# Kernel optimization log

Hardware: AMD Instinct MI355X
Metric: run time of the kernel (lower is better)

## Reference

```python
import jax, jax.numpy as jnp
import numpy as np

N = 2048      # num_nodes
B = 64        # batch
D_IN = 2      # input_dim per node
UNITS = 64    # hidden dim
K = 2         # max_diffusion_step
N_SUP = 2     # dual_random_walk -> two supports
M = N_SUP * K + 1           # num_matrices = 5
IN_SIZE = D_IN + UNITS      # 66
E = 65536                   # nnz per support


def setup_inputs() -> dict:
    key = jax.random.key(0)
    ks = jax.random.split(key, 10)
    inputs = jax.random.normal(ks[0], (B, N * D_IN), jnp.float32)
    state = jax.random.normal(ks[1], (B, N * UNITS), jnp.float32)
    edges1 = jax.random.randint(ks[2], (2, E), 0, N)
    vals1 = jax.random.uniform(ks[3], (E,), jnp.float32) / 32.0  # ~row-stochastic scale
    edges2 = jax.random.randint(ks[4], (2, E), 0, N)
    vals2 = jax.random.uniform(ks[5], (E,), jnp.float32) / 32.0
    W_gate = jax.random.normal(ks[6], (IN_SIZE * M, 2 * UNITS), jnp.float32) * 0.08
    b_gate = jnp.ones((2 * UNITS,), jnp.float32)  # bias_start=1.0 for gate
    W_cand = jax.random.normal(ks[7], (IN_SIZE * M, UNITS), jnp.float32) * 0.08
    b_cand = jnp.zeros((UNITS,), jnp.float32)
    return dict(inputs=inputs, state=state, edges1=edges1, vals1=vals1,
                edges2=edges2, vals2=vals2, W_gate=W_gate, b_gate=b_gate,
                W_cand=W_cand, b_cand=b_cand)


def _spmm(rows, cols, vals, x):
    # sparse [N,N] @ dense [N,F] via gather + segment_sum
    return jax.ops.segment_sum(x[cols] * vals[:, None], rows, num_segments=N)


def _dconv(inp, st, supports, W, b, out_dim):
    # inputs/state -> [B, N, F] concat, F = IN_SIZE
    x = jnp.concatenate([inp.reshape(B, N, -1), st.reshape(B, N, -1)], axis=2)
    f = x.shape[2]
    x0 = x.transpose(1, 2, 0).reshape(N, f * B)  # [N, F*B]
    xs = [x0]
    for (rows, cols, vals) in supports:
        x1 = _spmm(rows, cols, vals, x0)
        xs.append(x1)
        xk_1, xk_2 = x1, x0
        for _ in range(2, K + 1):  # Chebyshev recursion: x_k = 2 S x_{k-1} - x_{k-2}
            xk = 2.0 * _spmm(rows, cols, vals, xk_1) - xk_2
            xs.append(xk)
            xk_1, xk_2 = xk, xk_1
    xcat = jnp.stack(xs, 0).reshape(M, N, f, B)
    xcat = xcat.transpose(3, 1, 2, 0).reshape(B * N, f * M)  # [B*N, F*M]
    out = xcat @ W + b
    return out.reshape(B, N * out_dim)


def reference(inputs, state, edges1, vals1, edges2, vals2, W_gate, b_gate, W_cand, b_cand):
    supports = [(edges1[0], edges1[1], vals1), (edges2[0], edges2[1], vals2)]
    value = jax.nn.sigmoid(_dconv(inputs, state, supports, W_gate, b_gate, 2 * UNITS))
    value = value.reshape(B, N, 2 * UNITS)
    r = value[:, :, :UNITS].reshape(B, N * UNITS)
    u = value[:, :, UNITS:].reshape(B, N * UNITS)
    c = jnp.tanh(_dconv(inputs, r * state, supports, W_cand, b_cand, UNITS))
    new_state = u * state + (1.0 - u) * c
    return new_state
```

## Files before the change

kernel.cpp:

```cpp
#include <hip/hip_runtime.h>
#include <stdint.h>

#define NN 2048
#define EE 65536
#define APITCH 360
#define XSN ((size_t)NN*4096)
#define XIN ((size_t)NN*128)

typedef unsigned short u16;
typedef __bf16 bf16x8 __attribute__((ext_vector_type(8)));
typedef float f32x4 __attribute__((ext_vector_type(4)));
typedef float f32x2 __attribute__((ext_vector_type(2)));
typedef unsigned u32x4 __attribute__((ext_vector_type(4)));

__device__ __forceinline__ float bf2f(u16 h){ return __uint_as_float(((unsigned)h)<<16); }
__device__ __forceinline__ u16 f2bf(float f){
  unsigned u = __float_as_uint(f);
  u += 0x7fffu + ((u>>16)&1u);
  return (u16)(u>>16);
}
__device__ __forceinline__ float loadf(const void* p, size_t i, int bfflag){
  return bfflag ? bf2f(((const u16*)p)[i]) : ((const float*)p)[i];
}
__device__ __forceinline__ f32x2 up2(unsigned u){
  f32x2 r; r.x = __uint_as_float(u<<16); r.y = __uint_as_float(u & 0xffff0000u); return r;
}
__device__ __forceinline__ unsigned pk2(f32x2 t){
  return (unsigned)f2bf(t.x) | ((unsigned)f2bf(t.y)<<16);
}
__device__ __forceinline__ void accv(float v, u32x4 d, f32x2* a){
  f32x2 vv = {v, v};
  a[0] += vv*up2(d.x); a[1] += vv*up2(d.y);
  a[2] += vv*up2(d.z); a[3] += vv*up2(d.w);
}

__global__ void setup1_k(const unsigned* __restrict__ vals,
                         const int* __restrict__ e1, const int* __restrict__ e2,
                         int* __restrict__ cnt, int* __restrict__ flag){
  int b = blockIdx.x, tid = threadIdx.x;
  if (b == 0){
    if (tid < 64){
      unsigned lo = vals[tid] & 0xffffu;
      unsigned long long m = __ballot(lo >= 0x2800u && lo < 0x3D80u);
      if (tid==0) *flag = (__popcll(m) >= 32) ? 1 : 0;
    }
  } else if (b <= 256){
    atomicAdd(&cnt[e1[(b-1)*256 + tid]], 1);
  } else {
    atomicAdd(&cnt[2048 + e2[(b-257)*256 + tid]], 1);
  }
}

__global__ void scan2_k(const int* __restrict__ cntA, int* __restrict__ rpA, int* __restrict__ curA){
  __shared__ int s[1024];
  const int* cnt = cntA + blockIdx.x*2048;
  int* rp  = rpA  + blockIdx.x*2049;
  int* cur = curA + blockIdx.x*2048;
  int t = threadIdx.x;
  int c0 = cnt[2*t], c1 = cnt[2*t+1];
  int ps = c0 + c1;
  s[t] = ps;
  __syncthreads();
  for (int off=1; off<1024; off<<=1){
    int v = (t>=off) ? s[t-off] : 0;
    __syncthreads();
    s[t] += v;
    __syncthreads();
  }
  int excl = s[t] - ps;
  rp[2*t] = excl;  cur[2*t] = excl;
  rp[2*t+1] = excl + c0;  cur[2*t+1] = excl + c0;
  if (t==0) rp[2048] = EE;
}

__global__ void setup2_k(const int* __restrict__ e1, const void* __restrict__ v1,
                         const int* __restrict__ e2, const void* __restrict__ v2,
                         int* __restrict__ curA, int2* __restrict__ scvA,
                         const void* __restrict__ Wg, const void* __restrict__ Wc,
                         u16* __restrict__ Wfg, u16* __restrict__ Wfc,
                         const void* __restrict__ inp, const void* __restrict__ st,
                         u16* __restrict__ XSb, u16* __restrict__ XIb,
                         const int* __restrict__ flag){
  int b = blockIdx.x, tid = threadIdx.x;
  int bfflag = *flag;
  if (b < 512){
    const int* rows; const int* cols; const void* vals; int* cur; int2* scv; int e;
    if (b < 256){ rows=e1; cols=e1+EE; vals=v1; cur=curA; scv=scvA; e=b*256+tid; }
    else { rows=e2; cols=e2+EE; vals=v2; cur=curA+2048; scv=scvA+EE; e=(b-256)*256+tid; }
    int r = rows[e];
    int p = atomicAdd(&cur[r], 1);
    int2 cv; cv.x = cols[e] << 13; cv.y = __float_as_int(loadf(vals, e, bfflag));
    scv[p] = cv;
  } else if (b < 776){
    int bb = b - 512;
    const void* W; u16* Wf; int O, OT, i;
    if (bb < 176){ W=Wg; Wf=Wfg; O=128; OT=8; i=bb*256+tid; }
    else { W=Wc; Wf=Wfc; O=64; OT=4; i=(bb-176)*256+tid; }
    int j = i & 7, L = (i>>3)&63, tq = i>>9;
    int t = tq % OT, q = tq / OT;
    int o = t*16 + (L&15);
    int kk = q*32 + (L>>4)*8 + j;
    float v = 0.f;
    if (kk < 320){ int m = kk>>6, f = (kk&63)+2; v = loadf(W, (size_t)(f*5+m)*O + o, bfflag); }
    else if (kk < 330){ int tt = kk-320; int m = tt>>1, f = tt&1; v = loadf(W, (size_t)(f*5+m)*O + o, bfflag); }
    Wf[i] = f2bf(v);
  } else {
    int n = b - 776;
    if (bfflag){
      const uint4* sp = (const uint4*)st;
      uint4* xp = (uint4*)(XSb + (size_t)n*4096);
      #pragma unroll
      for (int it=0; it<2; ++it){
        int r = tid + it*256;
        int bb = r>>3, v4 = r&7;
        xp[r] = sp[(size_t)bb*(NN*8) + (size_t)n*8 + v4];
      }
      if (tid < 64){
        ((unsigned*)XIb)[n*64 + tid] = ((const unsigned*)inp)[(size_t)tid*NN + n];
      }
    } else {
      for (int i=tid; i<4096; i+=256){
        int bb=i>>6, f=i&63;
        XSb[(size_t)n*4096+i] = f2bf(((const float*)st)[(size_t)bb*(NN*64) + n*64 + f]);
      }
      for (int i=tid; i<128; i+=256){
        int bb=i>>1, f=i&1;
        XIb[(size_t)n*128+i] = f2bf(((const float*)inp)[(size_t)bb*(NN*2) + n*2 + f]);
      }
    }
  }
}

template<int CHEB>
__global__ __launch_bounds__(64) void spmm_k(
    u16* __restrict__ XSb, u16* __restrict__ XIb,
    const int* __restrict__ rpA, const int2* __restrict__ scvA){
  int sup = blockIdx.y;
  const int* rp = rpA + sup*2049;
  const int2* scv = scvA + sup*EE;
  const int srcm = CHEB ? (sup?3:1) : 0;
  const int dstm = CHEB ? (sup?4:2) : (sup?3:1);
  int tid = threadIdx.x;
  int bx = blockIdx.x;
  if (bx < NN*8){
    int ch = bx & 7, n = bx >> 3;
    int e0 = rp[n], e1 = rp[n+1];
    unsigned offB = (unsigned)(ch*64 + tid)*16;
    const char* srcp = (const char*)(XSb + (size_t)srcm*XSN) + offB;
    f32x2 a[4] = {{0.f,0.f},{0.f,0.f},{0.f,0.f},{0.f,0.f}};
    int e = e0;
    for (; e+7 < e1; e += 8){
      const int4* s4 = (const int4*)(scv + e);
      int4 p0 = s4[0], p1 = s4[1], p2 = s4[2], p3 = s4[3];
      u32x4 d0 = *(const u32x4*)(srcp + (unsigned)p0.x);
      u32x4 d1 = *(const u32x4*)(srcp + (unsigned)p0.z);
      u32x4 d2 = *(const u32x4*)(srcp + (unsigned)p1.x);
      u32x4 d3 = *(const u32x4*)(srcp + (unsigned)p1.z);
      u32x4 d4 = *(const u32x4*)(srcp + (unsigned)p2.x);
      u32x4 d5 = *(const u32x4*)(srcp + (unsigned)p2.z);
      u32x4 d6 = *(const u32x4*)(srcp + (unsigned)p3.x);
      u32x4 d7 = *(const u32x4*)(srcp + (unsigned)p3.z);
      accv(__int_as_float(p0.y), d0, a);
      accv(__int_as_float(p0.w), d1, a);
      accv(__int_as_float(p1.y), d2, a);
      accv(__int_as_float(p1.w), d3, a);
      accv(__int_as_float(p2.y), d4, a);
      accv(__int_as_float(p2.w), d5, a);
      accv(__int_as_float(p3.y), d6, a);
      accv(__int_as_float(p3.w), d7, a);
    }
    for (; e < e1; ++e){
      int2 c = scv[e];
      accv(__int_as_float(c.y), *(const u32x4*)(srcp + (unsigned)c.x), a);
    }
    unsigned doff = ((unsigned)n << 13) + offB;
    u32x4 w;
    if (CHEB){
      u32x4 o = *(const u32x4*)((const char*)XSb + doff);
      f32x2 t;
      t = 2.f*a[0] - up2(o.x); w.x = pk2(t);
      t = 2.f*a[1] - up2(o.y); w.y = pk2(t);
      t = 2.f*a[2] - up2(o.z); w.z = pk2(t);
      t = 2.f*a[3] - up2(o.w); w.w = pk2(t);
    } else {
      w.x = pk2(a[0]); w.y = pk2(a[1]); w.z = pk2(a[2]); w.w = pk2(a[3]);
    }
    *(u32x4*)((char*)(XSb + (size_t)dstm*XSN) + doff) = w;
  } else {
    int idx = bx - NN*8;
    int n = idx*2 + (tid>>5), m = tid & 31;
    int e0 = rp[n], e1 = rp[n+1];
    const char* srcp = (const char*)(XIb + (size_t)srcm*XIN) + m*8;
    f32x2 a0 = {0.f,0.f}, a1 = {0.f,0.f};
    for (int e=e0; e<e1; ++e){
      int2 cv = scv[e];
      uint2 d = *(const uint2*)(srcp + ((unsigned)cv.x >> 5));
      f32x2 vv = {__int_as_float(cv.y), __int_as_float(cv.y)};
      a0 += vv*up2(d.x); a1 += vv*up2(d.y);
    }
    unsigned doff = (unsigned)n*256 + m*8;
    if (CHEB){
      uint2 o = *(const uint2*)((const char*)XIb + doff);
      a0 = 2.f*a0 - up2(o.x); a1 = 2.f*a1 - up2(o.y);
    }
    uint2 wv; wv.x = pk2(a0); wv.y = pk2(a1);
    *(uint2*)((char*)(XIb + (size_t)dstm*XIN) + doff) = wv;
  }
}

template<int OT, int MODE>
__global__ __launch_bounds__(256) void gemm_k(
    u16* __restrict__ XSb, const u16* __restrict__ XIb,
    const u16* __restrict__ Wf, const void* __restrict__ bias,
    const void* __restrict__ state, void* __restrict__ outp,
    const int* __restrict__ flag){
  __shared__ __align__(16) u16 A[64*APITCH];
  int tid = threadIdx.x, n = blockIdx.x;
  int bfflag = *flag;
  #pragma unroll
  for (int m=0;m<5;m++){
    const uint4* src = (const uint4*)(XSb + (size_t)m*XSN + ((size_t)n<<12));
    #pragma unroll
    for (int it=0; it<2; ++it){
      int r = tid + it*256;
      uint4 d = src[r];
      int b = r>>3, f0 = (r&7)*8;
      *(uint4*)&A[b*APITCH + m*64 + f0] = d;
    }
  }
  for (int i=tid; i<320; i+=256){
    int m = i>>6, b = i&63;
    unsigned v = ((const unsigned*)XIb)[(size_t)m*(XIN/2) + n*64 + b];
    *(unsigned*)&A[b*APITCH + 320 + 2*m] = v;
  }
  for (int i=tid; i<64*15; i+=256){
    int b = i/15, j = i - b*15;
    *(unsigned*)&A[b*APITCH + 330 + 2*j] = 0;
  }
  const int TW = OT/4;
  int lane = tid & 63, w = tid >> 6;
  int m16 = lane & 15, q4 = lane >> 4;
  const bf16x8* wp = (const bf16x8*)Wf;
  bf16x8 wfr[11][TW];
  #pragma unroll
  for (int q=0;q<11;q++){
    #pragma unroll
    for (int i=0;i<TW;i++) wfr[q][i] = wp[(q*OT + (w + 4*i))*64 + lane];
  }
  __syncthreads();
  #pragma unroll
  for (int rt4=0; rt4<4; ++rt4){
    const u16* arow = A + (rt4*16 + m16)*APITCH + q4*8;
    f32x4 acc[TW];
    #pragma unroll
    for (int i=0;i<TW;i++) acc[i] = (f32x4){0.f,0.f,0.f,0.f};
    #pragma unroll
    for (int q=0;q<11;q++){
      bf16x8 af = *((const bf16x8*)(arow + q*32));
      #pragma unroll
      for (int i=0;i<TW;i++)
        acc[i] = __builtin_amdgcn_mfma_f32_16x16x32_bf16(af, wfr[q][i], acc[i], 0, 0, 0);
    }
    #pragma unroll
    for (int i=0;i<TW;i++){
      int t = w + 4*i;
      int o = t*16 + m16;
      float bo = loadf(bias, o, bfflag);
      #pragma unroll
      for (int r=0;r<4;r++){
        int b = rt4*16 + q4*4 + r;
        float x = acc[i][r] + bo;
        if (MODE==0){
          float s = 1.f/(1.f + __expf(-x));
          if (i==0){
            float st = loadf(state, (size_t)b*(NN*64) + (size_t)n*64 + o, bfflag);
            XSb[((size_t)n<<12) + b*64 + o] = f2bf(s*st);
          } else {
            size_t idx = (size_t)b*(NN*64) + (size_t)n*64 + (o-64);
            if (bfflag) ((u16*)outp)[idx] = f2bf(s); else ((float*)outp)[idx] = s;
          }
        } else {
          float c = tanhf(x);
          size_t idx = (size_t)b*(NN*64) + (size_t)n*64 + o;
          float uu = bfflag ? bf2f(((const u16*)outp)[idx]) : ((const float*)outp)[idx];
          float st = loadf(state, idx, bfflag);
          float ns = uu*st + (1.f-uu)*c;
          if (bfflag) ((u16*)outp)[idx] = f2bf(ns); else ((float*)outp)[idx] = ns;
        }
      }
    }
  }
}

extern "C" void kernel_launch(void* const* d_in, const int* in_sizes, int n_in,
                              void* d_out, int out_size, void* d_ws, size_t ws_size,
                              hipStream_t stream) {
  const void* inputs = d_in[0];
  const void* state  = d_in[1];
  const int* edges1 = (const int*)d_in[2];
  const void* vals1  = d_in[3];
  const int* edges2 = (const int*)d_in[4];
  const void* vals2  = d_in[5];
  const void* Wg     = d_in[6];
  const void* bg     = d_in[7];
  const void* Wc     = d_in[8];
  const void* bc     = d_in[9];

  char* ws = (char*)d_ws;
  size_t off = 0;
  auto get = [&](size_t bytes)->void*{
    void* p = ws + off; off = (off + bytes + 255) & ~(size_t)255; return p;
  };
  u16* XSb = (u16*)get(5*XSN*2);
  u16* XIb = (u16*)get(5*XIN*2);
  u16* Wfg = (u16*)get(11*8*64*8*2);
  u16* Wfc = (u16*)get(11*4*64*8*2);
  int* cnt  = (int*)get(2*2048*4);
  int* rp   = (int*)get(2*2049*4);
  int* cur  = (int*)get(2*2048*4);
  int* flag = (int*)get(4);
  int2* scv = (int2*)get((size_t)2*EE*8);

  hipMemsetAsync(cnt, 0, 2*2048*4, stream);
  setup1_k<<<513,256,0,stream>>>((const unsigned*)vals1, edges1, edges2, cnt, flag);
  scan2_k<<<2,1024,0,stream>>>(cnt, rp, cur);
  setup2_k<<<776+NN,256,0,stream>>>(edges1, vals1, edges2, vals2, cur, scv,
                                    Wg, Wc, Wfg, Wfc, inputs, state, XSb, XIb, flag);

  dim3 sg(NN*8 + NN/2, 2);
  spmm_k<0><<<sg,64,0,stream>>>(XSb, XIb, rp, scv);
  spmm_k<1><<<sg,64,0,stream>>>(XSb, XIb, rp, scv);
  gemm_k<8,0><<<NN,256,0,stream>>>(XSb, XIb, Wfg, bg, state, d_out, flag);
  spmm_k<0><<<sg,64,0,stream>>>(XSb, XIb, rp, scv);
  spmm_k<1><<<sg,64,0,stream>>>(XSb, XIb, rp, scv);
  gemm_k<4,1><<<NN,256,0,stream>>>(XSb, XIb, Wfc, bc, state, d_out, flag);
}
```

Baseline: 440.2 us.

## Fold Chebyshev recursion into GEMM weights and re-split gate/candidate GEMM kernels

Drops the 2*S*x - x0 Chebyshev combine from the second SpMM hop and folds it into the weights instead: W0 absorbs the -W2 and -W4 terms and W2/W4 are doubled. The second SpMM therefore no longer reads the earlier matrix, which saves memory traffic. The gate GEMM is rewritten to use 512 threads with one output tile per wave, and the candidate GEMM is split into two blocks per node so each thread holds fewer weight registers and more blocks run in parallel. The algebra is exact, but the rounding changes because the bf16 SpMM output is no longer combined in fp32 before being stored.

Measured after the change: 415.4 us. -5.6%, faster.

```diff
diff --git a/kernel.cpp b/kernel.cpp
--- a/kernel.cpp
+++ b/kernel.cpp
@@ -71,6 +71,17 @@
   rp[2*t] = excl;  cur[2*t] = excl;
   rp[2*t+1] = excl + c0;  cur[2*t+1] = excl + c0;
   if (t==0) rp[2048] = EE;
+}
+
+__device__ __forceinline__ float wfold(const void* W, int O, int m, int f, int o, int bfflag){
+  float v = loadf(W, (size_t)(f*5+m)*O + o, bfflag);
+  if (m == 0){
+    v -= loadf(W, (size_t)(f*5+2)*O + o, bfflag);
+    v -= loadf(W, (size_t)(f*5+4)*O + o, bfflag);
+  } else if (m == 2 || m == 4){
+    v *= 2.f;
+  }
+  return v;
 }
 
 __global__ void setup2_k(const int* __restrict__ e1, const void* __restrict__ v1,
@@ -101,8 +112,8 @@
     int o = t*16 + (L&15);
     int kk = q*32 + (L>>4)*8 + j;
     float v = 0.f;
-    if (kk < 320){ int m = kk>>6, f = (kk&63)+2; v = loadf(W, (size_t)(f*5+m)*O + o, bfflag); }
-    else if (kk < 330){ int tt = kk-320; int m = tt>>1, f = tt&1; v = loadf(W, (size_t)(f*5+m)*O + o, bfflag); }
+    if (kk < 320){ int m = kk>>6, f = (kk&63)+2; v = wfold(W, O, m, f, o, bfflag); }
+    else if (kk < 330){ int tt = kk-320; int m = tt>>1, f = tt&1; v = wfold(W, O, m, f, o, bfflag); }
     Wf[i] = f2bf(v);
   } else {
     int n = b - 776;
@@ -131,15 +142,15 @@
   }
 }
 
-template<int CHEB>
+template<int HOP>
 __global__ __launch_bounds__(64) void spmm_k(
     u16* __restrict__ XSb, u16* __restrict__ XIb,
     const int* __restrict__ rpA, const int2* __restrict__ scvA){
   int sup = blockIdx.y;
   const int* rp = rpA + sup*2049;
   const int2* scv = scvA + sup*EE;
-  const int srcm = CHEB ? (sup?3:1) : 0;
-  const int dstm = CHEB ? (sup?4:2) : (sup?3:1);
+  const int srcm = HOP ? (sup?3:1) : 0;
+  const int dstm = HOP ? (sup?4:2) : (sup?3:1);
   int tid = threadIdx.x;
   int bx = blockIdx.x;
   if (bx < NN*8){
@@ -175,16 +186,7 @@
     }
     unsigned doff = ((unsigned)n << 13) + offB;
     u32x4 w;
-    if (CHEB){
-      u32x4 o = *(const u32x4*)((const char*)XSb + doff);
-      f32x2 t;
-      t = 2.f*a[0] - up2(o.x); w.x = pk2(t);
-      t = 2.f*a[1] - up2(o.y); w.y = pk2(t);
-      t = 2.f*a[2] - up2(o.z); w.z = pk2(t);
-      t = 2.f*a[3] - up2(o.w); w.w = pk2(t);
-    } else {
-      w.x = pk2(a[0]); w.y = pk2(a[1]); w.z = pk2(a[2]); w.w = pk2(a[3]);
-    }
+    w.x = pk2(a[0]); w.y = pk2(a[1]); w.z = pk2(a[2]); w.w = pk2(a[3]);
     *(u32x4*)((char*)(XSb + (size_t)dstm*XSN) + doff) = w;
   } else {
     int idx = bx - NN*8;
@@ -199,17 +201,12 @@
       a0 += vv*up2(d.x); a1 += vv*up2(d.y);
     }
     unsigned doff = (unsigned)n*256 + m*8;
-    if (CHEB){
-      uint2 o = *(const uint2*)((const char*)XIb + doff);
-      a0 = 2.f*a0 - up2(o.x); a1 = 2.f*a1 - up2(o.y);
-    }
     uint2 wv; wv.x = pk2(a0); wv.y = pk2(a1);
     *(uint2*)((char*)(XIb + (size_t)dstm*XIN) + doff) = wv;
   }
 }
 
-template<int OT, int MODE>
-__global__ __launch_bounds__(256) void gemm_k(
+__global__ __launch_bounds__(512, 4) void gemm_gate_k(
     u16* __restrict__ XSb, const u16* __restrict__ XIb,
     const u16* __restrict__ Wf, const void* __restrict__ bias,
     const void* __restrict__ state, void* __restrict__ outp,
@@ -217,77 +214,113 @@
   __shared__ __align__(16) u16 A[64*APITCH];
   int tid = threadIdx.x, n = blockIdx.x;
   int bfflag = *flag;
-  #pragma unroll
-  for (int m=0;m<5;m++){
-    const uint4* src = (const uint4*)(XSb + (size_t)m*XSN + ((size_t)n<<12));
-    #pragma unroll
-    for (int it=0; it<2; ++it){
-      int r = tid + it*256;
-      uint4 d = src[r];
-      int b = r>>3, f0 = (r&7)*8;
+  {
+    int r = tid;
+    int b = r>>3, f0 = (r&7)*8;
+    #pragma unroll
+    for (int m=0;m<5;m++){
+      uint4 d = ((const uint4*)(XSb + (size_t)m*XSN + ((size_t)n<<12)))[r];
       *(uint4*)&A[b*APITCH + m*64 + f0] = d;
     }
   }
-  for (int i=tid; i<320; i+=256){
-    int m = i>>6, b = i&63;
+  if (tid < 320){
+    int m = tid>>6, b = tid&63;
     unsigned v = ((const unsigned*)XIb)[(size_t)m*(XIN/2) + n*64 + b];
     *(unsigned*)&A[b*APITCH + 320 + 2*m] = v;
   }
-  for (int i=tid; i<64*15; i+=256){
+  for (int i=tid; i<64*15; i+=512){
     int b = i/15, j = i - b*15;
     *(unsigned*)&A[b*APITCH + 330 + 2*j] = 0;
   }
-  const int TW = OT/4;
   int lane = tid & 63, w = tid >> 6;
   int m16 = lane & 15, q4 = lane >> 4;
   const bf16x8* wp = (const bf16x8*)Wf;
-  bf16x8 wfr[11][TW];
+  bf16x8 wfr[11];
   #pragma unroll
-  for (int q=0;q<11;q++){
-    #pragma unroll
-    for (int i=0;i<TW;i++) wfr[q][i] = wp[(q*OT + (w + 4*i))*64 + lane];
-  }
+  for (int q=0;q<11;q++) wfr[q] = wp[(q*8 + w)*64 + lane];
   __syncthreads();
+  int o = w*16 + m16;
+  float bo = loadf(bias, o, bfflag);
   #pragma unroll
   for (int rt4=0; rt4<4; ++rt4){
     const u16* arow = A + (rt4*16 + m16)*APITCH + q4*8;
-    f32x4 acc[TW];
-    #pragma unroll
-    for (int i=0;i<TW;i++) acc[i] = (f32x4){0.f,0.f,0.f,0.f};
+    f32x4 acc = (f32x4){0.f,0.f,0.f,0.f};
     #pragma unroll
     for (int q=0;q<11;q++){
       bf16x8 af = *((const bf16x8*)(arow + q*32));
-      #pragma unroll
-      for (int i=0;i<TW;i++)
-        acc[i] = __builtin_amdgcn_mfma_f32_16x16x32_bf16(af, wfr[q][i], acc[i], 0, 0, 0);
-    }
-    #pragma unroll
-    for (int i=0;i<TW;i++){
-      int t = w + 4*i;
-      int o = t*16 + m16;
-      float bo = loadf(bias, o, bfflag);
-      #pragma unroll
-      for (int r=0;r<4;r++){
-        int b = rt4*16 + q4*4 + r;
-        float x = acc[i][r] + bo;
-        if (MODE==0){
-          float s = 1.f/(1.f + __expf(-x));
-          if (i==0){
-            float st = loadf(state, (size_t)b*(NN*64) + (size_t)n*64 + o, bfflag);
-            XSb[((size_t)n<<12) + b*64 + o] = f2bf(s*st);
-          } else {
-            size_t idx = (size_t)b*(NN*64) + (size_t)n*64 + (o-64);
-            if (bfflag) ((u16*)outp)[idx] = f2bf(s); else ((float*)outp)[idx] = s;
-          }
-        } else {
-          float c = tanhf(x);
-          size_t idx = (size_t)b*(NN*64) + (size_t)n*64 + o;
-          float uu = bfflag ? bf2f(((const u16*)outp)[idx]) : ((const float*)outp)[idx];
-          float st = loadf(state, idx, bfflag);
-          float ns = uu*st + (1.f-uu)*c;
-          if (bfflag) ((u16*)outp)[idx] = f2bf(ns); else ((float*)outp)[idx] = ns;
-        }
-      }
+      acc = __builtin_amdgcn_mfma_f32_16x16x32_bf16(af, wfr[q], acc, 0, 0, 0);
+    }
+    #pragma unroll
+    for (int r=0;r<4;r++){
+      int b = rt4*16 + q4*4 + r;
+      float x = acc[r] + bo;
+      float s = 1.f/(1.f + __expf(-x));
+      if (w < 4){
+        float st = loadf(state, (size_t)b*(NN*64) + (size_t)n*64 + o, bfflag);
+        XSb[((size_t)n<<12) + b*64 + o] = f2bf(s*st);
+      } else {
+        size_t idx = (size_t)b*(NN*64) + (size_t)n*64 + (o-64);
+        if (bfflag) ((u16*)outp)[idx] = f2bf(s); else ((float*)outp)[idx] = s;
+      }
+    }
+  }
+}
+
+__global__ __launch_bounds__(256, 4) void gemm_cand_k(
+    u16* __restrict__ XSb, const u16* __restrict__ XIb,
+    const u16* __restrict__ Wf, const void* __restrict__ bias,
+    const void* __restrict__ state, void* __restrict__ outp,
+    const int* __restrict__ flag){
+  __shared__ __align__(16) u16 A[32*APITCH];
+  int tid = threadIdx.x;
+  int h = blockIdx.x & 1, n = blockIdx.x >> 1;
+  int bfflag = *flag;
+  {
+    int r = tid;
+    int bl = r>>3, f0 = (r&7)*8;
+    #pragma unroll
+    for (int m=0;m<5;m++){
+      uint4 d = ((const uint4*)(XSb + (size_t)m*XSN + ((size_t)n<<12)))[h*256 + r];
+      *(uint4*)&A[bl*APITCH + m*64 + f0] = d;
+    }
+  }
+  if (tid < 160){
+    int m = tid>>5, bl = tid&31;
+    unsigned v = ((const unsigned*)XIb)[(size_t)m*(XIN/2) + n*64 + h*32 + bl];
+    *(unsigned*)&A[bl*APITCH + 320 + 2*m] = v;
+  }
+  for (int i=tid; i<32*15; i+=256){
+    int bl = i/15, j = i - bl*15;
+    *(unsigned*)&A[bl*APITCH + 330 + 2*j] = 0;
+  }
+  int lane = tid & 63, w = tid >> 6;
+  int m16 = lane & 15, q4 = lane >> 4;
+  const bf16x8* wp = (const bf16x8*)Wf;
+  bf16x8 wfr[11];
+  #pragma unroll
+  for (int q=0;q<11;q++) wfr[q] = wp[(q*4 + w)*64 + lane];
+  __syncthreads();
+  int o = w*16 + m16;
+  float bo = loadf(bias, o, bfflag);
+  #pragma unroll
+  for (int rt2=0; rt2<2; ++rt2){
+    const u16* arow = A + (rt2*16 + m16)*APITCH + q4*8;
+    f32x4 acc = (f32x4){0.f,0.f,0.f,0.f};
+    #pragma unroll
+    for (int q=0;q<11;q++){
+      bf16x8 af = *((const bf16x8*)(arow + q*32));
+      acc = __builtin_amdgcn_mfma_f32_16x16x32_bf16(af, wfr[q], acc, 0, 0, 0);
+    }
+    #pragma unroll
+    for (int r=0;r<4;r++){
+      int b = h*32 + rt2*16 + q4*4 + r;
+      float x = acc[r] + bo;
+      float c = tanhf(x);
+      size_t idx = (size_t)b*(NN*64) + (size_t)n*64 + o;
+      float uu = bfflag ? bf2f(((const u16*)outp)[idx]) : ((const float*)outp)[idx];
+      float st = loadf(state, idx, bfflag);
+      float ns = uu*st + (1.f-uu)*c;
+      if (bfflag) ((u16*)outp)[idx] = f2bf(ns); else ((float*)outp)[idx] = ns;
     }
   }
 }
@@ -330,8 +363,8 @@
   dim3 sg(NN*8 + NN/2, 2);
   spmm_k<0><<<sg,64,0,stream>>>(XSb, XIb, rp, scv);
   spmm_k<1><<<sg,64,0,stream>>>(XSb, XIb, rp, scv);
-  gemm_k<8,0><<<NN,256,0,stream>>>(XSb, XIb, Wfg, bg, state, d_out, flag);
+  gemm_gate_k<<<NN,512,0,stream>>>(XSb, XIb, Wfg, bg, state, d_out, flag);
   spmm_k<0><<<sg,64,0,stream>>>(XSb, XIb, rp, scv);
   spmm_k<1><<<sg,64,0,stream>>>(XSb, XIb, rp, scv);
-  gemm_k<4,1><<<NN,256,0,stream>>>(XSb, XIb, Wfc, bc, state, d_out, flag);
-}
+  gemm_cand_k<<<NN*2,256,0,stream>>>(XSb, XIb, Wfc, bc, state, d_out, flag);
+}
```
